# Kernel optimization log

Hardware: AMD Instinct MI355X
Metric: run time of the kernel (lower is better)

Reference implementation:

```python
import jax, jax.numpy as jnp
import numpy as np

NUM_NODES = 100000
EMB_DIM = 64
OUT_C = 64
K = 3
NUM_EDGES = 1600000


def setup_inputs() -> dict:
    key = jax.random.key(0)
    k1, k2, k3, k4 = jax.random.split(key, 4)
    x_indices = jnp.arange(NUM_NODES, dtype=jnp.int64)
    ei = jax.random.randint(k1, (2, NUM_EDGES), 0, NUM_NODES, dtype=jnp.int64)
    # learned params: embedding table + final linear of SGConv
    emb_weight = jax.random.normal(k2, (NUM_NODES, EMB_DIM), dtype=jnp.float32)
    lin_w = jax.random.normal(k3, (OUT_C, EMB_DIM), dtype=jnp.float32) / np.sqrt(EMB_DIM)
    lin_b = jax.random.normal(k4, (OUT_C,), dtype=jnp.float32) * 0.01
    return {"x_indices": x_indices, "ei": ei, "emb_weight": emb_weight,
            "lin_w": lin_w, "lin_b": lin_b}


def _sgconv(x, ei, lin_w, lin_b, k_hops):
    """PyG SGConv: (D^-1/2 (A+I) D^-1/2)^K X, then Linear."""
    n = x.shape[0]
    row, col = ei[0], ei[1]
    loops = jnp.arange(n, dtype=ei.dtype)
    row = jnp.concatenate([row, loops])
    col = jnp.concatenate([col, loops])
    ones = jnp.ones(row.shape[0], dtype=x.dtype)
    deg = jax.ops.segment_sum(ones, col, num_segments=n)  # in-degree incl. self-loops
    dinv = jnp.where(deg > 0, jax.lax.rsqrt(deg), 0.0)
    norm = dinv[row] * dinv[col]  # [E+N]
    for _ in range(k_hops):
        # gather source features, scale, scatter-add to targets
        x = jax.ops.segment_sum(x[row] * norm[:, None], col, num_segments=n)
    return x @ lin_w.T + lin_b


def reference(x_indices, ei, emb_weight, lin_w, lin_b):
    x = emb_weight[x_indices]  # [N, EMB_DIM] embedding lookup
    return _sgconv(x, ei, lin_w, lin_b, K)
```

## Files before the change

### kernel.cpp

```cpp
#include <hip/hip_runtime.h>
#include <hip/hip_bf16.h>
#include <math.h>


#define FLAG_MX 0
#define FLAG_ME 1
#define SH 9
#define WC 512
#define CH 4096

using short8 = __attribute__((ext_vector_type(8))) short;
using f32x4 = __attribute__((ext_vector_type(4))) float;

__device__ inline int idx_at(const void* p, long long i, int mode) {
    switch (mode) {
        case 1: return (int)((const long long*)p)[i];
        case 2: return (int)((const float*)p)[i];
        case 3: return (int)((const double*)p)[i];
        default: return ((const int*)p)[i];
    }
}

__device__ inline unsigned short f2bf(float f) {
    union { float f; unsigned u; } v; v.f = f;
    unsigned r = v.u + 0x7FFFu + ((v.u >> 16) & 1u);
    return (unsigned short)(r >> 16);
}
__device__ inline float bflo(unsigned d) { union { unsigned u; float f; } v; v.u = d << 16; return v.f; }
__device__ inline float bfhi(unsigned d) { union { unsigned u; float f; } v; v.u = d & 0xFFFF0000u; return v.f; }
__device__ inline unsigned pk(float a, float b) {
    return (unsigned)f2bf(a) | ((unsigned)f2bf(b) << 16);
}

__device__ int detect_me_block(const void* ei, int n, int* sbuf) {
    int t = threadIdx.x;
    int oke = 15;
    const int* w = (const int*)ei;
    const long long* L = (const long long*)ei;
    const float* f = (const float*)ei;
    const double* d = (const double*)ei;
    for (int k = t; k < 2048; k += 256) {
        if (!((unsigned)w[k] < (unsigned)n)) oke &= ~1;
        long long lv = L[k];
        if (!(lv >= 0 && lv < (long long)n)) oke &= ~2;
        float fv = f[k];
        if (!(fv >= 0.f && fv < (float)n && fv == truncf(fv))) oke &= ~4;
        double dv = d[k];
        if (!(dv >= 0.0 && dv < (double)n && dv == trunc(dv))) oke &= ~8;
    }
    sbuf[t] = oke;
    __syncthreads();
    for (int st = 128; st; st >>= 1) {
        if (t < st) sbuf[t] &= sbuf[t + st];
        __syncthreads();
    }
    int r = sbuf[0];
    __syncthreads();
    return (r & 2) ? 1 : (r & 8) ? 3 : (r & 4) ? 2 : 0;
}

__device__ int detect_mx_block(const void* xidx, int* sbuf) {
    int t = threadIdx.x;
    int okx = 15;
    const int* w = (const int*)xidx;
    const long long* L = (const long long*)xidx;
    const float* f = (const float*)xidx;
    const double* d = (const double*)xidx;
    for (int k = t; k < 2048; k += 256) {
        if (w[k] != k) okx &= ~1;
        if (L[k] != (long long)k) okx &= ~2;
        if (!(f[k] == (float)k)) okx &= ~4;
        if (!(d[k] == (double)k)) okx &= ~8;
    }
    sbuf[t] = okx;
    __syncthreads();
    for (int st = 128; st; st >>= 1) {
        if (t < st) sbuf[t] &= sbuf[t + st];
        __syncthreads();
    }
    int r = sbuf[0];
    __syncthreads();
    return (r & 2) ? 1 : (r & 8) ? 3 : (r & 4) ? 2 : 0;
}

__global__ void __launch_bounds__(256) k_p1(
        const void* __restrict__ ei, const void* __restrict__ xidx,
        long long E, int n, int NBUK, int NBLK,
        int* __restrict__ bhist, int* __restrict__ flags) {
    __shared__ int hist[256];
    __shared__ int sbuf[256];
    int t = threadIdx.x;
    int blk = blockIdx.x;
    int me = detect_me_block(ei, n, sbuf);
    if (blk == 0) {
        int mx = detect_mx_block(xidx, sbuf);
        if (t == 0) { flags[FLAG_ME] = me; flags[FLAG_MX] = mx; }
    }
    long long base = (long long)blk * CH;
    int cnt = (int)min((long long)CH, E - base);
    hist[t] = 0;
    __syncthreads();
    for (int i = t; i < cnt; i += 256) {
        int c = idx_at(ei, E + base + i, me);
        int b = min(c >> SH, NBUK - 1);
        atomicAdd(&hist[b], 1);
    }
    __syncthreads();
    if (t < NBUK) bhist[(size_t)t * NBLK + blk] = hist[t];
}

__global__ void __launch_bounds__(256) k_p2a(
        int* __restrict__ bhist, int* __restrict__ gcount, int NBLK) {
    __shared__ int s[256];
    int b = blockIdx.x;
    int t = threadIdx.x;
    int* row = bhist + (size_t)b * NBLK;
    int carry = 0;
    for (int base = 0; base < NBLK; base += 256) {
        int i = base + t;
        int v = (i < NBLK) ? row[i] : 0;
        s[t] = v;
        __syncthreads();
        for (int st = 1; st < 256; st <<= 1) {
            int add = (t >= st) ? s[t - st] : 0;
            __syncthreads();
            s[t] += add;
            __syncthreads();
        }
        if (i < NBLK) row[i] = carry + s[t] - v;
        int total = s[255];
        __syncthreads();
        carry += total;
    }
    if (t == 0) gcount[b] = carry;
}

__global__ void k_p2b(const int* gcount, int* gbase, int NBUK, int* off, int n) {
    __shared__ int s[256];
    int t = threadIdx.x;
    int v = (t < NBUK) ? gcount[t] : 0;
    s[t] = v;
    __syncthreads();
    for (int st = 1; st < 256; st <<= 1) {
        int add = (t >= st) ? s[t - st] : 0;
        __syncthreads();
        s[t] += add;
        __syncthreads();
    }
    if (t < NBUK) gbase[t] = s[t] - v;
    if (t == NBUK - 1) { gbase[NBUK] = s[t]; off[n] = s[t]; }
}

__global__ void __launch_bounds__(256) k_p3(
        const void* __restrict__ ei, long long E, int n, int NBUK, int NBLK,
        const int* __restrict__ bhist, const int* __restrict__ gbase,
        uint2* __restrict__ gstag, const int* __restrict__ flags) {
    __shared__ int hist[256], lbase[256], rsv[256], lcur[256], s[256];
    __shared__ uint2 stage[CH];
    int t = threadIdx.x;
    int blk = blockIdx.x;
    long long base = (long long)blk * CH;
    int cnt = (int)min((long long)CH, E - base);
    int me = flags[FLAG_ME];
    hist[t] = 0;
    __syncthreads();
    for (int i = t; i < cnt; i += 256) {
        int c = idx_at(ei, E + base + i, me);
        atomicAdd(&hist[min(c >> SH, NBUK - 1)], 1);
    }
    __syncthreads();
    int v = hist[t];
    s[t] = v;
    __syncthreads();
    for (int st = 1; st < 256; st <<= 1) {
        int add = (t >= st) ? s[t - st] : 0;
        __syncthreads();
        s[t] += add;
        __syncthreads();
    }
    lbase[t] = s[t] - v;
    lcur[t] = s[t] - v;
    if (t < NBUK) rsv[t] = gbase[t] + bhist[(size_t)t * NBLK + blk];
    __syncthreads();
    for (int i = t; i < cnt; i += 256) {
        long long e = base + i;
        int r = idx_at(ei, e, me);
        int c = idx_at(ei, E + e, me);
        int b = min(c >> SH, NBUK - 1);
        int slot = atomicAdd(&lcur[b], 1);
        stage[slot] = make_uint2((unsigned)r, (unsigned)c);
    }
    __syncthreads();
    for (int i = t; i < cnt; i += 256) {
        uint2 e = stage[i];
        int b = min((int)(e.y >> SH), NBUK - 1);
        gstag[rsv[b] + (i - lbase[b])] = e;
    }
}

__global__ void __launch_bounds__(256) k_p4(
        const uint2* __restrict__ gstag, const int* __restrict__ gbase,
        int* __restrict__ off, float* __restrict__ dinv,
        int* __restrict__ rowidx, int n) {
    __shared__ int hist[WC], lofs[WC], cur[WC], p[256];
    int t = threadIdx.x;
    int b = blockIdx.x;
    int cbase = b << SH;
    int e0 = gbase[b], e1 = gbase[b + 1];
    int cnt = e1 - e0;
    hist[t] = 0; hist[t + 256] = 0;
    __syncthreads();
    for (int i = t; i < cnt; i += 256) {
        int cl = (int)gstag[e0 + i].y - cbase;
        cl = min(max(cl, 0), WC - 1);
        atomicAdd(&hist[cl], 1);
    }
    __syncthreads();
    int a0 = hist[2 * t], a1 = hist[2 * t + 1];
    int s2 = a0 + a1;
    p[t] = s2;
    __syncthreads();
    for (int st = 1; st < 256; st <<= 1) {
        int add = (t >= st) ? p[t - st] : 0;
        __syncthreads();
        p[t] += add;
        __syncthreads();
    }
    int excl = p[t] - s2;
    lofs[2 * t] = excl;       cur[2 * t] = excl;
    lofs[2 * t + 1] = excl + a0; cur[2 * t + 1] = excl + a0;
    __syncthreads();
    for (int j = t; j < WC; j += 256) {
        int c = cbase + j;
        if (c < n) {
            off[c] = e0 + lofs[j];
            dinv[c] = rsqrtf((float)(hist[j] + 1));
        }
    }
    for (int i = t; i < cnt; i += 256) {
        uint2 e = gstag[e0 + i];
        int cl = min(max((int)e.y - cbase, 0), WC - 1);
        int slot = atomicAdd(&cur[cl], 1);
        rowidx[e0 + slot] = (int)e.x;
    }
}

__global__ void __launch_bounds__(256) k_z0(
        const void* __restrict__ xidx, const float4* __restrict__ emb4,
        const float* __restrict__ dinv, uint4* __restrict__ z, int n,
        const int* __restrict__ flags) {
    int i = blockIdx.x * 256 + threadIdx.x;
    if (i >= n * 8) return;
    int node = i >> 3, q = i & 7;
    int xi = idx_at(xidx, node, flags[FLAG_MX]);
    if ((unsigned)xi >= (unsigned)n) xi = 0;
    float d = dinv[node];
    float4 a = emb4[(long long)xi * 16 + q * 2];
    float4 b = emb4[(long long)xi * 16 + q * 2 + 1];
    uint4 o;
    o.x = pk(a.x * d, a.y * d);
    o.y = pk(a.z * d, a.w * d);
    o.z = pk(b.x * d, b.y * d);
    o.w = pk(b.z * d, b.w * d);
    z[(long long)node * 8 + q] = o;
}

__device__ inline void acc8(float* acc, uint4 s) {
    acc[0] += bflo(s.x); acc[1] += bfhi(s.x);
    acc[2] += bflo(s.y); acc[3] += bfhi(s.y);
    acc[4] += bflo(s.z); acc[5] += bfhi(s.z);
    acc[6] += bflo(s.w); acc[7] += bfhi(s.w);
}

__global__ void __launch_bounds__(256) k_hop(
        const uint4* __restrict__ zin, uint4* __restrict__ zout,
        const float* __restrict__ dinv, const int* __restrict__ off,
        const int* __restrict__ rowidx, int n, int last) {
    int tid = blockIdx.x * 256 + threadIdx.x;
    int node = tid >> 3;
    int q = tid & 3;
    q = tid & 7;
    if (node >= n) return;
    float acc[8];
    {
        uint4 s = zin[(long long)node * 8 + q];
        acc[0] = bflo(s.x); acc[1] = bfhi(s.x);
        acc[2] = bflo(s.y); acc[3] = bfhi(s.y);
        acc[4] = bflo(s.z); acc[5] = bfhi(s.z);
        acc[6] = bflo(s.w); acc[7] = bfhi(s.w);
    }
    int e0 = off[node], e1 = off[node + 1];
    int e = e0;
    for (; e + 4 <= e1; e += 4) {
        int r0 = rowidx[e + 0];
        int r1 = rowidx[e + 1];
        int r2 = rowidx[e + 2];
        int r3 = rowidx[e + 3];
        uint4 s0 = zin[(long long)r0 * 8 + q];
        uint4 s1 = zin[(long long)r1 * 8 + q];
        uint4 s2 = zin[(long long)r2 * 8 + q];
        uint4 s3 = zin[(long long)r3 * 8 + q];
        acc8(acc, s0);
        acc8(acc, s1);
        acc8(acc, s2);
        acc8(acc, s3);
    }
    for (; e < e1; e++) {
        int r = rowidx[e];
        acc8(acc, zin[(long long)r * 8 + q]);
    }
    float d = dinv[node];
    float sc = last ? d : d * d;
    uint4 o;
    o.x = pk(acc[0] * sc, acc[1] * sc);
    o.y = pk(acc[2] * sc, acc[3] * sc);
    o.z = pk(acc[4] * sc, acc[5] * sc);
    o.w = pk(acc[6] * sc, acc[7] * sc);
    zout[(long long)node * 8 + q] = o;
}

__global__ void __launch_bounds__(256) k_lin_mfma(
        const short8* __restrict__ x8, const float* __restrict__ w,
        const float* __restrict__ b, float* __restrict__ out, int n, int ntiles) {
    int lane = threadIdx.x & 63;
    int wv = threadIdx.x >> 6;
    int col = lane & 15, quad = lane >> 4;

    short8 bw[4][2];
#pragma unroll
    for (int tN = 0; tN < 4; tN++)
#pragma unroll
        for (int s = 0; s < 2; s++) {
            const float* src = w + (tN * 16 + col) * 64 + s * 32 + quad * 8;
            short8 v;
#pragma unroll
            for (int j = 0; j < 8; j++) v[j] = (short)f2bf(src[j]);
            bw[tN][s] = v;
        }
    float bv[4];
#pragma unroll
    for (int tN = 0; tN < 4; tN++) bv[tN] = b[tN * 16 + col];

    int tile = blockIdx.x * 4 + wv;
    if (tile >= ntiles) return;
    int node0 = tile * 16;

    short8 a[2];
    int m = node0 + col;
#pragma unroll
    for (int s = 0; s < 2; s++) {
        if (m < n) a[s] = x8[(size_t)m * 8 + s * 4 + quad];
        else a[s] = short8{0, 0, 0, 0, 0, 0, 0, 0};
    }
#pragma unroll
    for (int tN = 0; tN < 4; tN++) {
        f32x4 acc = {bv[tN], bv[tN], bv[tN], bv[tN]};
        acc = __builtin_amdgcn_mfma_f32_16x16x32_bf16(a[0], bw[tN][0], acc, 0, 0, 0);
        acc = __builtin_amdgcn_mfma_f32_16x16x32_bf16(a[1], bw[tN][1], acc, 0, 0, 0);
#pragma unroll
        for (int r = 0; r < 4; r++) {
            int node = node0 + quad * 4 + r;
            if (node < n) out[(size_t)node * 64 + tN * 16 + col] = acc[r];
        }
    }
}

extern "C" void kernel_launch(void* const* d_in, const int* in_sizes, int n_in,
                              void* d_out, int out_size, void* d_ws, size_t ws_size,
                              hipStream_t stream) {
    const void* xidx = d_in[0];
    const void* ei = d_in[1];
    const float* emb = (const float*)d_in[2];
    const float* w = (const float*)d_in[3];
    const float* b = (const float*)d_in[4];

    const int n = in_sizes[0];
    const long long E = in_sizes[1] / 2;
    int NBUK = (int)((n + WC - 1) >> SH);
    if (NBUK > 256) NBUK = 256;
    const int NBLK = (int)((E + CH - 1) / CH);

    char* p = (char*)d_ws;
    auto alloc = [&](size_t bytes) -> void* {
        void* r = (void*)p;
        p += (bytes + 255) & ~(size_t)255;
        return r;
    };
    int* flags = (int*)alloc(256);
    float* dinv = (float*)alloc((size_t)n * 4);
    int* off = (int*)alloc((size_t)(n + 1) * 4);
    int* gcount = (int*)alloc(257 * 4);
    int* gbase = (int*)alloc(258 * 4);
    int* bhist = (int*)alloc((size_t)NBLK * NBUK * 4);
    int* rowidx = (int*)alloc((size_t)E * 4);
    uint4* zA = (uint4*)alloc((size_t)n * 64 * 2);
    uint4* zS = (uint4*)d_out;

    uint2* gstag;
    if ((size_t)E * 8 <= (size_t)n * 64 * 2)
        gstag = (uint2*)((char*)d_out + (size_t)n * 64 * 2);
    else
        gstag = (uint2*)alloc((size_t)E * 8);

    k_p1<<<NBLK, 256, 0, stream>>>(ei, xidx, E, n, NBUK, NBLK, bhist, flags);
    k_p2a<<<NBUK, 256, 0, stream>>>(bhist, gcount, NBLK);
    k_p2b<<<1, 256, 0, stream>>>(gcount, gbase, NBUK, off, n);
    k_p3<<<NBLK, 256, 0, stream>>>(ei, E, n, NBUK, NBLK, bhist, gbase, gstag, flags);
    k_p4<<<NBUK, 256, 0, stream>>>(gstag, gbase, off, dinv, rowidx, n);

    const int gZ = (n * 8 + 255) / 256;
    const int ntiles = (n + 15) / 16;
    const int gM = (ntiles + 3) / 4;

    k_z0<<<gZ, 256, 0, stream>>>(xidx, (const float4*)emb, dinv, zS, n, flags);
    k_hop<<<gZ, 256, 0, stream>>>(zS, zA, dinv, off, rowidx, n, 0);
    k_hop<<<gZ, 256, 0, stream>>>(zA, zS, dinv, off, rowidx, n, 0);
    k_hop<<<gZ, 256, 0, stream>>>(zS, zA, dinv, off, rowidx, n, 1);
    k_lin_mfma<<<gM, 256, 0, stream>>>((const short8*)zA, w, b, (float*)d_out,
                                       n, ntiles);
}
```

Measured before the change: 264.6 us.

## Pack staged edges into 32 bits and degree-sort nodes within buckets for hops

Staged edges are packed into one 32-bit word (23-bit row, 9-bit local column) instead of a uint2, which halves staging traffic and shared memory in the partition kernels. The scatter pass finds each edge's bucket by binary search over local bases. Within each 512-node bucket, nodes are counting-sorted by in-degree into slot arrays (node, offset, degree), so wavefronts in the hop kernels process nodes of similar degree and diverge less. The hop inner loop is unrolled to 8 gathers with a 2-wide tail. In exchange it adds three slot arrays, an extra indirection per node, and a 23-bit limit on row index.

```diff
diff --git a/kernel.cpp b/kernel.cpp
--- a/kernel.cpp
+++ b/kernel.cpp
@@ -8,6 +8,7 @@
 #define SH 9
 #define WC 512
 #define CH 4096
+#define RMASK 0x7FFFFFu
 
 using short8 = __attribute__((ext_vector_type(8))) short;
 using f32x4 = __attribute__((ext_vector_type(4))) float;
@@ -135,7 +136,7 @@
     if (t == 0) gcount[b] = carry;
 }
 
-__global__ void k_p2b(const int* gcount, int* gbase, int NBUK, int* off, int n) {
+__global__ void k_p2b(const int* gcount, int* gbase, int NBUK) {
     __shared__ int s[256];
     int t = threadIdx.x;
     int v = (t < NBUK) ? gcount[t] : 0;
@@ -148,15 +149,15 @@
         __syncthreads();
     }
     if (t < NBUK) gbase[t] = s[t] - v;
-    if (t == NBUK - 1) { gbase[NBUK] = s[t]; off[n] = s[t]; }
+    if (t == NBUK - 1) gbase[NBUK] = s[t];
 }
 
 __global__ void __launch_bounds__(256) k_p3(
         const void* __restrict__ ei, long long E, int n, int NBUK, int NBLK,
         const int* __restrict__ bhist, const int* __restrict__ gbase,
-        uint2* __restrict__ gstag, const int* __restrict__ flags) {
+        unsigned* __restrict__ gstag, const int* __restrict__ flags) {
     __shared__ int hist[256], lbase[256], rsv[256], lcur[256], s[256];
-    __shared__ uint2 stage[CH];
+    __shared__ unsigned stage[CH];
     int t = threadIdx.x;
     int blk = blockIdx.x;
     long long base = (long long)blk * CH;
@@ -187,32 +188,40 @@
         int r = idx_at(ei, e, me);
         int c = idx_at(ei, E + e, me);
         int b = min(c >> SH, NBUK - 1);
+        unsigned pkv = ((unsigned)r & RMASK) |
+                       (((unsigned)(c - (b << SH)) & (WC - 1)) << 23);
         int slot = atomicAdd(&lcur[b], 1);
-        stage[slot] = make_uint2((unsigned)r, (unsigned)c);
-    }
-    __syncthreads();
-    for (int i = t; i < cnt; i += 256) {
-        uint2 e = stage[i];
-        int b = min((int)(e.y >> SH), NBUK - 1);
-        gstag[rsv[b] + (i - lbase[b])] = e;
+        stage[slot] = pkv;
+    }
+    __syncthreads();
+    for (int i = t; i < cnt; i += 256) {
+        unsigned pkv = stage[i];
+        int lo = 0, hi = NBUK - 1;
+        while (lo < hi) {
+            int mid = (lo + hi + 1) >> 1;
+            if (lbase[mid] <= i) lo = mid; else hi = mid - 1;
+        }
+        gstag[rsv[lo] + (i - lbase[lo])] = pkv;
     }
 }
 
 __global__ void __launch_bounds__(256) k_p4(
-        const uint2* __restrict__ gstag, const int* __restrict__ gbase,
-        int* __restrict__ off, float* __restrict__ dinv,
-        int* __restrict__ rowidx, int n) {
+        const unsigned* __restrict__ gstag, const int* __restrict__ gbase,
+        float* __restrict__ dinv, int* __restrict__ rowidx,
+        int* __restrict__ nodep, int* __restrict__ offp, int* __restrict__ degp,
+        int n) {
     __shared__ int hist[WC], lofs[WC], cur[WC], p[256];
+    __shared__ int dcnt[64], dbase[64];
     int t = threadIdx.x;
     int b = blockIdx.x;
     int cbase = b << SH;
     int e0 = gbase[b], e1 = gbase[b + 1];
     int cnt = e1 - e0;
     hist[t] = 0; hist[t + 256] = 0;
-    __syncthreads();
-    for (int i = t; i < cnt; i += 256) {
-        int cl = (int)gstag[e0 + i].y - cbase;
-        cl = min(max(cl, 0), WC - 1);
+    if (t < 64) dcnt[t] = 0;
+    __syncthreads();
+    for (int i = t; i < cnt; i += 256) {
+        int cl = (int)(gstag[e0 + i] >> 23);
         atomicAdd(&hist[cl], 1);
     }
     __syncthreads();
@@ -230,18 +239,36 @@
     lofs[2 * t] = excl;       cur[2 * t] = excl;
     lofs[2 * t + 1] = excl + a0; cur[2 * t + 1] = excl + a0;
     __syncthreads();
-    for (int j = t; j < WC; j += 256) {
-        int c = cbase + j;
-        if (c < n) {
-            off[c] = e0 + lofs[j];
-            dinv[c] = rsqrtf((float)(hist[j] + 1));
-        }
-    }
-    for (int i = t; i < cnt; i += 256) {
-        uint2 e = gstag[e0 + i];
-        int cl = min(max((int)e.y - cbase, 0), WC - 1);
+    int ncols = n - cbase;
+    if (ncols < 0) ncols = 0;
+    if (ncols > WC) ncols = WC;
+    for (int j = t; j < ncols; j += 256) {
+        dinv[cbase + j] = rsqrtf((float)(hist[j] + 1));
+        atomicAdd(&dcnt[min(hist[j], 63)], 1);
+    }
+    for (int j = ncols + t; j < WC; j += 256) {
+        int s = b * WC + j;
+        nodep[s] = -1; degp[s] = 0; offp[s] = 0;
+    }
+    __syncthreads();
+    if (t == 0) {
+        int run = 0;
+        for (int d = 0; d < 64; d++) { dbase[d] = run; run += dcnt[d]; }
+    }
+    __syncthreads();
+    for (int j = t; j < ncols; j += 256) {
+        int d = min(hist[j], 63);
+        int r = atomicAdd(&dbase[d], 1);
+        int s = b * WC + r;
+        nodep[s] = cbase + j;
+        offp[s] = e0 + lofs[j];
+        degp[s] = hist[j];
+    }
+    for (int i = t; i < cnt; i += 256) {
+        unsigned pkv = gstag[e0 + i];
+        int cl = (int)(pkv >> 23);
         int slot = atomicAdd(&cur[cl], 1);
-        rowidx[e0 + slot] = (int)e.x;
+        rowidx[e0 + slot] = (int)(pkv & RMASK);
     }
 }
 
@@ -274,13 +301,15 @@
 
 __global__ void __launch_bounds__(256) k_hop(
         const uint4* __restrict__ zin, uint4* __restrict__ zout,
-        const float* __restrict__ dinv, const int* __restrict__ off,
-        const int* __restrict__ rowidx, int n, int last) {
+        const float* __restrict__ dinv, const int* __restrict__ rowidx,
+        const int* __restrict__ nodep, const int* __restrict__ offp,
+        const int* __restrict__ degp, int n, int nslots, int last) {
     int tid = blockIdx.x * 256 + threadIdx.x;
-    int node = tid >> 3;
-    int q = tid & 3;
-    q = tid & 7;
-    if (node >= n) return;
+    int slot = tid >> 3;
+    int q = tid & 7;
+    if (slot >= nslots) return;
+    int node = nodep[slot];
+    if ((unsigned)node >= (unsigned)n) return;
     float acc[8];
     {
         uint4 s = zin[(long long)node * 8 + q];
@@ -289,26 +318,31 @@
         acc[4] = bflo(s.z); acc[5] = bfhi(s.z);
         acc[6] = bflo(s.w); acc[7] = bfhi(s.w);
     }
-    int e0 = off[node], e1 = off[node + 1];
-    int e = e0;
-    for (; e + 4 <= e1; e += 4) {
-        int r0 = rowidx[e + 0];
-        int r1 = rowidx[e + 1];
-        int r2 = rowidx[e + 2];
-        int r3 = rowidx[e + 3];
+    int e = offp[slot];
+    int e1 = e + degp[slot];
+    for (; e + 8 <= e1; e += 8) {
+        int r0 = rowidx[e + 0], r1 = rowidx[e + 1];
+        int r2 = rowidx[e + 2], r3 = rowidx[e + 3];
+        int r4 = rowidx[e + 4], r5 = rowidx[e + 5];
+        int r6 = rowidx[e + 6], r7 = rowidx[e + 7];
         uint4 s0 = zin[(long long)r0 * 8 + q];
         uint4 s1 = zin[(long long)r1 * 8 + q];
         uint4 s2 = zin[(long long)r2 * 8 + q];
         uint4 s3 = zin[(long long)r3 * 8 + q];
-        acc8(acc, s0);
-        acc8(acc, s1);
-        acc8(acc, s2);
-        acc8(acc, s3);
-    }
-    for (; e < e1; e++) {
-        int r = rowidx[e];
-        acc8(acc, zin[(long long)r * 8 + q]);
-    }
+        uint4 s4 = zin[(long long)r4 * 8 + q];
+        uint4 s5 = zin[(long long)r5 * 8 + q];
+        uint4 s6 = zin[(long long)r6 * 8 + q];
+        uint4 s7 = zin[(long long)r7 * 8 + q];
+        acc8(acc, s0); acc8(acc, s1); acc8(acc, s2); acc8(acc, s3);
+        acc8(acc, s4); acc8(acc, s5); acc8(acc, s6); acc8(acc, s7);
+    }
+    for (; e + 2 <= e1; e += 2) {
+        int r0 = rowidx[e], r1 = rowidx[e + 1];
+        uint4 s0 = zin[(long long)r0 * 8 + q];
+        uint4 s1 = zin[(long long)r1 * 8 + q];
+        acc8(acc, s0); acc8(acc, s1);
+    }
+    for (; e < e1; e++) acc8(acc, zin[(long long)rowidx[e] * 8 + q]);
     float d = dinv[node];
     float sc = last ? d : d * d;
     uint4 o;
@@ -379,6 +413,7 @@
     int NBUK = (int)((n + WC - 1) >> SH);
     if (NBUK > 256) NBUK = 256;
     const int NBLK = (int)((E + CH - 1) / CH);
+    const int nslots = NBUK * WC;
 
     char* p = (char*)d_ws;
     auto alloc = [&](size_t bytes) -> void* {
@@ -388,34 +423,37 @@
     };
     int* flags = (int*)alloc(256);
     float* dinv = (float*)alloc((size_t)n * 4);
-    int* off = (int*)alloc((size_t)(n + 1) * 4);
     int* gcount = (int*)alloc(257 * 4);
     int* gbase = (int*)alloc(258 * 4);
     int* bhist = (int*)alloc((size_t)NBLK * NBUK * 4);
     int* rowidx = (int*)alloc((size_t)E * 4);
+    int* nodep = (int*)alloc((size_t)nslots * 4);
+    int* offp = (int*)alloc((size_t)nslots * 4);
+    int* degp = (int*)alloc((size_t)nslots * 4);
     uint4* zA = (uint4*)alloc((size_t)n * 64 * 2);
     uint4* zS = (uint4*)d_out;
 
-    uint2* gstag;
-    if ((size_t)E * 8 <= (size_t)n * 64 * 2)
-        gstag = (uint2*)((char*)d_out + (size_t)n * 64 * 2);
+    unsigned* gstag;
+    if ((size_t)E * 4 <= (size_t)n * 64 * 2)
+        gstag = (unsigned*)((char*)d_out + (size_t)n * 64 * 2);
     else
-        gstag = (uint2*)alloc((size_t)E * 8);
+        gstag = (unsigned*)alloc((size_t)E * 4);
 
     k_p1<<<NBLK, 256, 0, stream>>>(ei, xidx, E, n, NBUK, NBLK, bhist, flags);
     k_p2a<<<NBUK, 256, 0, stream>>>(bhist, gcount, NBLK);
-    k_p2b<<<1, 256, 0, stream>>>(gcount, gbase, NBUK, off, n);
+    k_p2b<<<1, 256, 0, stream>>>(gcount, gbase, NBUK);
     k_p3<<<NBLK, 256, 0, stream>>>(ei, E, n, NBUK, NBLK, bhist, gbase, gstag, flags);
-    k_p4<<<NBUK, 256, 0, stream>>>(gstag, gbase, off, dinv, rowidx, n);
+    k_p4<<<NBUK, 256, 0, stream>>>(gstag, gbase, dinv, rowidx, nodep, offp, degp, n);
 
     const int gZ = (n * 8 + 255) / 256;
+    const int gH = (nslots * 8 + 255) / 256;
     const int ntiles = (n + 15) / 16;
     const int gM = (ntiles + 3) / 4;
 
     k_z0<<<gZ, 256, 0, stream>>>(xidx, (const float4*)emb, dinv, zS, n, flags);
-    k_hop<<<gZ, 256, 0, stream>>>(zS, zA, dinv, off, rowidx, n, 0);
-    k_hop<<<gZ, 256, 0, stream>>>(zA, zS, dinv, off, rowidx, n, 0);
-    k_hop<<<gZ, 256, 0, stream>>>(zS, zA, dinv, off, rowidx, n, 1);
+    k_hop<<<gH, 256, 0, stream>>>(zS, zA, dinv, rowidx, nodep, offp, degp, n, nslots, 0);
+    k_hop<<<gH, 256, 0, stream>>>(zA, zS, dinv, rowidx, nodep, offp, degp, n, nslots, 0);
+    k_hop<<<gH, 256, 0, stream>>>(zS, zA, dinv, rowidx, nodep, offp, degp, n, nslots, 1);
     k_lin_mfma<<<gM, 256, 0, stream>>>((const short8*)zA, w, b, (float*)d_out,
                                        n, ntiles);
 }
```

New measurement: 286.1 us. 1.08x slower.

## Pack staged edges to 32 bits and fuse scan and embedding init into CSR build

Applied to the files above, without the earlier changes.

Staged edges are now packed into one 32-bit word (23-bit source row plus 9-bit local column), which halves the scatter staging traffic in the bucket pass and the CSR pass. The single-block global scan kernel is removed and each block recomputes the small bucket-offset scan itself. The embedding lookup with degree scaling is folded into the CSR-build kernel, so two launches are removed. The trade-offs are redundant per-block scans, a binary search per staged edge in the scatter loop, a limit of 2^23 nodes on row indices, and less parallelism for the embedding init, which now runs on only NBUK blocks.

```diff
diff --git a/kernel.cpp b/kernel.cpp
--- a/kernel.cpp
+++ b/kernel.cpp
@@ -8,6 +8,7 @@
 #define SH 9
 #define WC 512
 #define CH 4096
+#define RMASK 0x7FFFFFu
 
 using short8 = __attribute__((ext_vector_type(8))) short;
 using f32x4 = __attribute__((ext_vector_type(4))) float;
@@ -135,30 +136,30 @@
     if (t == 0) gcount[b] = carry;
 }
 
-__global__ void k_p2b(const int* gcount, int* gbase, int NBUK, int* off, int n) {
-    __shared__ int s[256];
+__device__ void scan_gcount(const int* gcount, int NBUK, int* p, int* gb_ex) {
     int t = threadIdx.x;
     int v = (t < NBUK) ? gcount[t] : 0;
-    s[t] = v;
+    p[t] = v;
     __syncthreads();
     for (int st = 1; st < 256; st <<= 1) {
-        int add = (t >= st) ? s[t - st] : 0;
-        __syncthreads();
-        s[t] += add;
-        __syncthreads();
-    }
-    if (t < NBUK) gbase[t] = s[t] - v;
-    if (t == NBUK - 1) { gbase[NBUK] = s[t]; off[n] = s[t]; }
+        int add = (t >= st) ? p[t - st] : 0;
+        __syncthreads();
+        p[t] += add;
+        __syncthreads();
+    }
+    gb_ex[t] = p[t] - v;
+    __syncthreads();
 }
 
 __global__ void __launch_bounds__(256) k_p3(
         const void* __restrict__ ei, long long E, int n, int NBUK, int NBLK,
-        const int* __restrict__ bhist, const int* __restrict__ gbase,
-        uint2* __restrict__ gstag, const int* __restrict__ flags) {
-    __shared__ int hist[256], lbase[256], rsv[256], lcur[256], s[256];
-    __shared__ uint2 stage[CH];
+        const int* __restrict__ bhist, const int* __restrict__ gcount,
+        unsigned* __restrict__ gstag, const int* __restrict__ flags) {
+    __shared__ int hist[256], lbase[256], rsv[256], lcur[256], s[256], gb[256];
+    __shared__ unsigned stage[CH];
     int t = threadIdx.x;
     int blk = blockIdx.x;
+    scan_gcount(gcount, NBUK, s, gb);
     long long base = (long long)blk * CH;
     int cnt = (int)min((long long)CH, E - base);
     int me = flags[FLAG_ME];
@@ -180,39 +181,49 @@
     }
     lbase[t] = s[t] - v;
     lcur[t] = s[t] - v;
-    if (t < NBUK) rsv[t] = gbase[t] + bhist[(size_t)t * NBLK + blk];
+    if (t < NBUK) rsv[t] = gb[t] + bhist[(size_t)t * NBLK + blk];
     __syncthreads();
     for (int i = t; i < cnt; i += 256) {
         long long e = base + i;
         int r = idx_at(ei, e, me);
         int c = idx_at(ei, E + e, me);
         int b = min(c >> SH, NBUK - 1);
+        unsigned pkv = ((unsigned)r & RMASK) |
+                       (((unsigned)(c - (b << SH)) & (WC - 1)) << 23);
         int slot = atomicAdd(&lcur[b], 1);
-        stage[slot] = make_uint2((unsigned)r, (unsigned)c);
-    }
-    __syncthreads();
-    for (int i = t; i < cnt; i += 256) {
-        uint2 e = stage[i];
-        int b = min((int)(e.y >> SH), NBUK - 1);
-        gstag[rsv[b] + (i - lbase[b])] = e;
+        stage[slot] = pkv;
+    }
+    __syncthreads();
+    for (int i = t; i < cnt; i += 256) {
+        unsigned pkv = stage[i];
+        int lo = 0, hi = NBUK - 1;
+        while (lo < hi) {
+            int mid = (lo + hi + 1) >> 1;
+            if (lbase[mid] <= i) lo = mid; else hi = mid - 1;
+        }
+        gstag[rsv[lo] + (i - lbase[lo])] = pkv;
     }
 }
 
 __global__ void __launch_bounds__(256) k_p4(
-        const uint2* __restrict__ gstag, const int* __restrict__ gbase,
+        const unsigned* __restrict__ gstag, const int* __restrict__ gcount,
         int* __restrict__ off, float* __restrict__ dinv,
-        int* __restrict__ rowidx, int n) {
-    __shared__ int hist[WC], lofs[WC], cur[WC], p[256];
+        int* __restrict__ rowidx, const void* __restrict__ xidx,
+        const float4* __restrict__ emb4, uint4* __restrict__ zS,
+        const int* __restrict__ flags, int n, int NBUK, long long E) {
+    __shared__ int hist[WC], lofs[WC], cur[WC], p[256], gb[256];
     int t = threadIdx.x;
     int b = blockIdx.x;
     int cbase = b << SH;
-    int e0 = gbase[b], e1 = gbase[b + 1];
+    scan_gcount(gcount, NBUK, p, gb);
+    int e0 = gb[b];
+    int e1 = e0 + gcount[b];
     int cnt = e1 - e0;
+    if (b == NBUK - 1 && t == 0) off[n] = e1;
     hist[t] = 0; hist[t + 256] = 0;
     __syncthreads();
     for (int i = t; i < cnt; i += 256) {
-        int cl = (int)gstag[e0 + i].y - cbase;
-        cl = min(max(cl, 0), WC - 1);
+        int cl = (int)(gstag[e0 + i] >> 23);
         atomicAdd(&hist[cl], 1);
     }
     __syncthreads();
@@ -230,39 +241,35 @@
     lofs[2 * t] = excl;       cur[2 * t] = excl;
     lofs[2 * t + 1] = excl + a0; cur[2 * t + 1] = excl + a0;
     __syncthreads();
-    for (int j = t; j < WC; j += 256) {
-        int c = cbase + j;
-        if (c < n) {
-            off[c] = e0 + lofs[j];
-            dinv[c] = rsqrtf((float)(hist[j] + 1));
-        }
-    }
-    for (int i = t; i < cnt; i += 256) {
-        uint2 e = gstag[e0 + i];
-        int cl = min(max((int)e.y - cbase, 0), WC - 1);
+    int ncols = n - cbase;
+    if (ncols < 0) ncols = 0;
+    if (ncols > WC) ncols = WC;
+    for (int j = t; j < ncols; j += 256) {
+        off[cbase + j] = e0 + lofs[j];
+        dinv[cbase + j] = rsqrtf((float)(hist[j] + 1));
+    }
+    for (int i = t; i < cnt; i += 256) {
+        unsigned pkv = gstag[e0 + i];
+        int cl = (int)(pkv >> 23);
         int slot = atomicAdd(&cur[cl], 1);
-        rowidx[e0 + slot] = (int)e.x;
-    }
-}
-
-__global__ void __launch_bounds__(256) k_z0(
-        const void* __restrict__ xidx, const float4* __restrict__ emb4,
-        const float* __restrict__ dinv, uint4* __restrict__ z, int n,
-        const int* __restrict__ flags) {
-    int i = blockIdx.x * 256 + threadIdx.x;
-    if (i >= n * 8) return;
-    int node = i >> 3, q = i & 7;
-    int xi = idx_at(xidx, node, flags[FLAG_MX]);
-    if ((unsigned)xi >= (unsigned)n) xi = 0;
-    float d = dinv[node];
-    float4 a = emb4[(long long)xi * 16 + q * 2];
-    float4 b = emb4[(long long)xi * 16 + q * 2 + 1];
-    uint4 o;
-    o.x = pk(a.x * d, a.y * d);
-    o.y = pk(a.z * d, a.w * d);
-    o.z = pk(b.x * d, b.y * d);
-    o.w = pk(b.z * d, b.w * d);
-    z[(long long)node * 8 + q] = o;
+        rowidx[e0 + slot] = (int)(pkv & RMASK);
+    }
+    int mx = flags[FLAG_MX];
+    for (int i = t; i < ncols * 8; i += 256) {
+        int j = i >> 3, q = i & 7;
+        int node = cbase + j;
+        int xi = idx_at(xidx, node, mx);
+        if ((unsigned)xi >= (unsigned)n) xi = 0;
+        float dv = rsqrtf((float)(hist[j] + 1));
+        float4 a = emb4[(long long)xi * 16 + q * 2];
+        float4 bb = emb4[(long long)xi * 16 + q * 2 + 1];
+        uint4 o;
+        o.x = pk(a.x * dv, a.y * dv);
+        o.y = pk(a.z * dv, a.w * dv);
+        o.z = pk(bb.x * dv, bb.y * dv);
+        o.w = pk(bb.z * dv, bb.w * dv);
+        zS[(long long)node * 8 + q] = o;
+    }
 }
 
 __device__ inline void acc8(float* acc, uint4 s) {
@@ -278,8 +285,7 @@
         const int* __restrict__ rowidx, int n, int last) {
     int tid = blockIdx.x * 256 + threadIdx.x;
     int node = tid >> 3;
-    int q = tid & 3;
-    q = tid & 7;
+    int q = tid & 7;
     if (node >= n) return;
     float acc[8];
     {
@@ -390,32 +396,30 @@
     float* dinv = (float*)alloc((size_t)n * 4);
     int* off = (int*)alloc((size_t)(n + 1) * 4);
     int* gcount = (int*)alloc(257 * 4);
-    int* gbase = (int*)alloc(258 * 4);
     int* bhist = (int*)alloc((size_t)NBLK * NBUK * 4);
     int* rowidx = (int*)alloc((size_t)E * 4);
     uint4* zA = (uint4*)alloc((size_t)n * 64 * 2);
     uint4* zS = (uint4*)d_out;
 
-    uint2* gstag;
-    if ((size_t)E * 8 <= (size_t)n * 64 * 2)
-        gstag = (uint2*)((char*)d_out + (size_t)n * 64 * 2);
+    unsigned* gstag;
+    if ((size_t)E * 4 <= (size_t)n * 64 * 2)
+        gstag = (unsigned*)((char*)d_out + (size_t)n * 64 * 2);
     else
-        gstag = (uint2*)alloc((size_t)E * 8);
+        gstag = (unsigned*)alloc((size_t)E * 4);
 
     k_p1<<<NBLK, 256, 0, stream>>>(ei, xidx, E, n, NBUK, NBLK, bhist, flags);
     k_p2a<<<NBUK, 256, 0, stream>>>(bhist, gcount, NBLK);
-    k_p2b<<<1, 256, 0, stream>>>(gcount, gbase, NBUK, off, n);
-    k_p3<<<NBLK, 256, 0, stream>>>(ei, E, n, NBUK, NBLK, bhist, gbase, gstag, flags);
-    k_p4<<<NBUK, 256, 0, stream>>>(gstag, gbase, off, dinv, rowidx, n);
-
-    const int gZ = (n * 8 + 255) / 256;
+    k_p3<<<NBLK, 256, 0, stream>>>(ei, E, n, NBUK, NBLK, bhist, gcount, gstag, flags);
+    k_p4<<<NBUK, 256, 0, stream>>>(gstag, gcount, off, dinv, rowidx, xidx,
+                                   (const float4*)emb, zS, flags, n, NBUK, E);
+
+    const int gF = (n * 8 + 255) / 256;
     const int ntiles = (n + 15) / 16;
     const int gM = (ntiles + 3) / 4;
 
-    k_z0<<<gZ, 256, 0, stream>>>(xidx, (const float4*)emb, dinv, zS, n, flags);
-    k_hop<<<gZ, 256, 0, stream>>>(zS, zA, dinv, off, rowidx, n, 0);
-    k_hop<<<gZ, 256, 0, stream>>>(zA, zS, dinv, off, rowidx, n, 0);
-    k_hop<<<gZ, 256, 0, stream>>>(zS, zA, dinv, off, rowidx, n, 1);
+    k_hop<<<gF, 256, 0, stream>>>(zS, zA, dinv, off, rowidx, n, 0);
+    k_hop<<<gF, 256, 0, stream>>>(zA, zS, dinv, off, rowidx, n, 0);
+    k_hop<<<gF, 256, 0, stream>>>(zS, zA, dinv, off, rowidx, n, 1);
     k_lin_mfma<<<gM, 256, 0, stream>>>((const short8*)zA, w, b, (float*)d_out,
                                        n, ntiles);
 }
```

Result: slower. 282.7 us (+6.8%).
